# Performance work log

Measured on AMD Instinct MI355X. Metric: run time of the kernel, lower is better.

## Reference

```python
import jax, jax.numpy as jnp
import numpy as np

SCALING = 16.0 / 8.0  # alpha / rank
GAMMA = 1.0
EPS = 1e-12


def setup_inputs() -> dict:
    key = jax.random.key(0)
    ks = jax.random.split(key, 8)
    B, T, H, O = 4, 2048, 4096, 4096
    E_tot, E_act, r = 16, 4, 8
    return {
        "x": jax.random.normal(ks[0], (B, T, H), jnp.float32),
        "W_base": jax.random.normal(ks[1], (O, H), jnp.float32) * 0.02,
        "b_base": jax.random.normal(ks[2], (O,), jnp.float32) * 0.02,
        "lora_A": jax.random.normal(ks[3], (E_tot, r, H), jnp.float32) * 0.02,
        "lora_B": jax.random.normal(ks[4], (E_tot, O, r), jnp.float32) * 0.02,
        "router_W": jax.random.normal(ks[5], (E_tot, H), jnp.float32) * 0.02,
        "router_b": jax.random.normal(ks[6], (E_tot,), jnp.float32) * 0.02,
        "domain_prior": jax.random.uniform(ks[7], (E_tot,), jnp.float32),
        "active": jnp.arange(E_act, dtype=jnp.int32),
    }


def reference(x, W_base, b_base, lora_A, lora_B, router_W, router_b, domain_prior, active):
    # Base linear: [B,T,H] @ [H,O] -> [B,T,O]
    y = jnp.einsum('bth,oh->bto', x, W_base) + b_base
    # Gather active experts' low-rank factors
    A = lora_A[active]   # [E, r, H]
    Bm = lora_B[active]  # [E, O, r]
    # Grouped low-rank GEMMs (dropout is identity at inference)
    z = jnp.einsum('bth,erh->bter', x, A)            # [B,T,E,r]
    contribs = jnp.einsum('bter,eor->bteo', z, Bm) * SCALING  # [B,T,E,O]
    # Token router logits over all experts, restricted to active set
    logits = jnp.einsum('bth,eh->bte', x, router_W) + router_b  # [B,T,E_tot]
    logits = logits[..., active]                                 # [B,T,E]
    prior = domain_prior[active]                                 # [E]
    alpha = jax.nn.softmax(jnp.log(prior + EPS) + logits / GAMMA, axis=-1)  # [B,T,E]
    return y + jnp.einsum('bteo,bte->bto', contribs, alpha)
```

## Files before the change

### kernel.cpp

```cpp
#include <hip/hip_runtime.h>
#include <hip/hip_bf16.h>


typedef _Float16 f16x8 __attribute__((ext_vector_type(8)));
typedef float    f32x4 __attribute__((ext_vector_type(4)));

constexpr int H  = 4096;
constexpr int O  = 4096;
constexpr int KP = 4160;
constexpr int EA = 4;
constexpr float SCALING_F = 2.0f;

typedef const __attribute__((address_space(1))) void gvoid;
typedef __attribute__((address_space(3))) void svoid;

__device__ inline void gload16(const void* g, void* s) {
  __builtin_amdgcn_global_load_lds((gvoid*)g, (svoid*)s, 16, 0, 0);
}

__global__ __launch_bounds__(256) void convert_w3_kernel(
    const float* __restrict__ W, const float* __restrict__ lora_B,
    const float* __restrict__ lora_A, const float* __restrict__ router_W,
    const int* __restrict__ active, _Float16* __restrict__ wh,
    _Float16* __restrict__ vh) {
  const int bid = blockIdx.x;
  const int tid = threadIdx.x;
  if (bid < O) {
    const int o = bid;
    const float* wrow = W + (size_t)o * H;
    _Float16* dstrow = wh + (size_t)o * KP;
    for (int g = tid; g < 520; g += 256) {
      const int k = g * 8;
      float v[8];
      if (k < H) {
        float4 a = *(const float4*)(wrow + k), b = *(const float4*)(wrow + k + 4);
        v[0] = a.x; v[1] = a.y; v[2] = a.z; v[3] = a.w;
        v[4] = b.x; v[5] = b.y; v[6] = b.z; v[7] = b.w;
      } else if (k < H + 32) {
        const int e = (k - H) >> 3;
        const float* s = lora_B + ((size_t)active[e] * O + o) * 8;
        float4 a = *(const float4*)s, b = *(const float4*)(s + 4);
        v[0] = a.x; v[1] = a.y; v[2] = a.z; v[3] = a.w;
        v[4] = b.x; v[5] = b.y; v[6] = b.z; v[7] = b.w;
      } else {
#pragma unroll
        for (int i = 0; i < 8; ++i) v[i] = 0.f;
      }
      f16x8 h;
#pragma unroll
      for (int i = 0; i < 8; ++i) h[i] = (_Float16)v[i];
      *(f16x8*)(dstrow + k) = h;
    }
  } else {
    const int j = bid - O;
    const float* src = nullptr;
    if (j < 32)      src = lora_A + (size_t)(active[j >> 3] * 8 + (j & 7)) * H;
    else if (j < 36) src = router_W + (size_t)active[j - 32] * H;
    _Float16* dstrow = vh + (size_t)j * H;
    for (int g = tid; g < 512; g += 256) {
      const int k = g * 8;
      f16x8 h;
      if (src) {
        float4 a = *(const float4*)(src + k), b = *(const float4*)(src + k + 4);
        h[0] = (_Float16)a.x; h[1] = (_Float16)a.y;
        h[2] = (_Float16)a.z; h[3] = (_Float16)a.w;
        h[4] = (_Float16)b.x; h[5] = (_Float16)b.y;
        h[6] = (_Float16)b.z; h[7] = (_Float16)b.w;
      } else {
#pragma unroll
        for (int i = 0; i < 8; ++i) h[i] = (_Float16)0.f;
      }
      *(f16x8*)(dstrow + k) = h;
    }
  }
}

constexpr int RW5 = 16;

__global__ __launch_bounds__(1024) void router_fused5_kernel(
    const float* __restrict__ x, const _Float16* __restrict__ vh,
    const float* __restrict__ router_b, const float* __restrict__ prior,
    const int* __restrict__ active, _Float16* __restrict__ xh) {
  __shared__ float zred[RW5][16][48];
  const int tid  = threadIdx.x;
  const int lane = tid & 63;
  const int w    = tid >> 6;
  const long t0  = (long)blockIdx.x * 16;
  const int r15  = lane & 15;
  const int kg   = lane >> 4;

  const float*    xp  = x  + (t0 + r15) * H  + w * 256 + kg * 8;
  _Float16*       xhp = xh + (t0 + r15) * KP + w * 256 + kg * 8;
  const _Float16* vp  = vh + (size_t)r15 * H + w * 256 + kg * 8;

  f32x4 acc[3];
  const f32x4 zero = {0.f, 0.f, 0.f, 0.f};
  acc[0] = zero; acc[1] = zero; acc[2] = zero;

#pragma unroll
  for (int c = 0; c < 8; ++c) {
    const int ko = c * 32;
    float4 v0 = *(const float4*)(xp + ko);
    float4 v1 = *(const float4*)(xp + ko + 4);
    f16x8 a;
    a[0] = (_Float16)v0.x; a[1] = (_Float16)v0.y;
    a[2] = (_Float16)v0.z; a[3] = (_Float16)v0.w;
    a[4] = (_Float16)v1.x; a[5] = (_Float16)v1.y;
    a[6] = (_Float16)v1.z; a[7] = (_Float16)v1.w;
    *(f16x8*)(xhp + ko) = a;
#pragma unroll
    for (int nf = 0; nf < 3; ++nf) {
      f16x8 b = *(const f16x8*)(vp + (size_t)nf * 16 * H + ko);
      acc[nf] = __builtin_amdgcn_mfma_f32_16x16x32_f16(a, b, acc[nf], 0, 0, 0);
    }
  }

#pragma unroll
  for (int nf = 0; nf < 3; ++nf)
#pragma unroll
    for (int r = 0; r < 4; ++r)
      zred[w][kg * 4 + r][nf * 16 + r15] = acc[nf][r];
  __syncthreads();

  float s = 0.f;
  int tt = 0, jj = 0;
  if (tid < 16 * 48) {
    tt = tid / 48; jj = tid % 48;
#pragma unroll
    for (int ww = 0; ww < RW5; ++ww) s += zred[ww][tt][jj];
  }
  __syncthreads();
  if (tid < 16 * 48) zred[0][tt][jj] = s;
  __syncthreads();

  if (tid < 16 * EA) {
    const int t2 = tid >> 2, e = tid & 3;
    const float* zt = &zred[0][t2][0];
    float le[EA], mx = -1e30f;
#pragma unroll
    for (int e2 = 0; e2 < EA; ++e2) {
      const int ae = active[e2];
      le[e2] = logf(prior[ae] + 1e-12f) + zt[32 + e2] + router_b[ae];
      mx = fmaxf(mx, le[e2]);
    }
    float sum = 0.f;
#pragma unroll
    for (int e2 = 0; e2 < EA; ++e2) sum += expf(le[e2] - mx);
    const float a = expf(le[e] - mx) / sum * SCALING_F;
    f16x8 ch, zz;
#pragma unroll
    for (int r = 0; r < 8; ++r) {
      ch[r] = (_Float16)(a * zt[e * 8 + r]);
      zz[r] = (_Float16)0.f;
    }
    _Float16* xr = xh + (t0 + t2) * KP + H;
    *(f16x8*)(xr + e * 8) = ch;
    *(f16x8*)(xr + 32 + e * 8) = zz;
  }
}

constexpr int BM = 256, BN = 256, BK = 64, NT = KP / BK;

__global__ __launch_bounds__(512, 2) void gemm_kernel(
    const _Float16* __restrict__ xh, const _Float16* __restrict__ wh,
    const float* __restrict__ b_base, float* __restrict__ out) {
  __shared__ _Float16 As[2][BM * BK];
  __shared__ _Float16 Ws[2][BN * BK];
  const int tid  = threadIdx.x;
  const int lane = tid & 63;
  const int wave = tid >> 6;
  const int bid  = (int)blockIdx.x;
  const int im = bid >> 4;
  const int in = bid & 15;
  const size_t trow0 = (size_t)im * BM;
  const size_t ocol0 = (size_t)in * BN;
  const int wr = wave >> 2;
  const int wc = wave & 3;
  const int r15 = lane & 15;
  const int kg  = lane >> 4;

  f32x4 acc[8][4];
  const f32x4 zero = {0.f, 0.f, 0.f, 0.f};
#pragma unroll
  for (int m = 0; m < 8; ++m)
#pragma unroll
    for (int n = 0; n < 4; ++n) acc[m][n] = zero;

  auto stageA = [&](int s, int t, int h) {
#pragma unroll
    for (int i = 0; i < 2; ++i) {
      const int idx = tid + 512 * i;
      const int row = idx >> 3;
      const int sg  = (idx & 7) ^ (row & 7);
      gload16(xh + (trow0 + h * 128 + row) * KP + t * 64 + sg * 8,
              &As[s][h * 8192 + idx * 8]);
    }
  };
  auto stageB = [&](int s, int t, int h) {
#pragma unroll
    for (int i = 0; i < 2; ++i) {
      const int idx = tid + 512 * i;
      const int row = idx >> 3;
      const int sg  = (idx & 7) ^ (row & 7);
      gload16(wh + (ocol0 + h * 128 + row) * KP + t * 64 + sg * 8,
              &Ws[s][h * 8192 + idx * 8]);
    }
  };

  stageA(0, 0, 0); stageA(0, 0, 1);
  stageB(0, 0, 0); stageB(0, 0, 1);
  asm volatile("s_waitcnt vmcnt(0)" ::: "memory");
  __builtin_amdgcn_s_barrier();

  for (int t = 0; t < NT; ++t) {
    const int s = t & 1;
    const _Float16* Ab = &As[s][0];
    const _Float16* Bb = &Ws[s][0];
#pragma unroll
    for (int q = 0; q < 4; ++q) {
      const int mh = q >> 1, nh = q & 1;
      f16x8 af[4][2], bf[2][2];
#pragma unroll
      for (int m = 0; m < 4; ++m) {
        const int row = wr * 128 + (mh * 4 + m) * 16 + r15;
#pragma unroll
        for (int kk = 0; kk < 2; ++kk) {
          const int slot = (kk * 4 + kg) ^ (row & 7);
          af[m][kk] = *(const f16x8*)(Ab + row * 64 + slot * 8);
        }
      }
#pragma unroll
      for (int n = 0; n < 2; ++n) {
        const int row = wc * 64 + (nh * 2 + n) * 16 + r15;
#pragma unroll
        for (int kk = 0; kk < 2; ++kk) {
          const int slot = (kk * 4 + kg) ^ (row & 7);
          bf[n][kk] = *(const f16x8*)(Bb + row * 64 + slot * 8);
        }
      }
      if (t + 1 < NT) {
        if (q == 0)      { stageA(s ^ 1, t + 1, 0); stageA(s ^ 1, t + 1, 1); }
        else if (q == 1) { stageB(s ^ 1, t + 1, 0); stageB(s ^ 1, t + 1, 1); }
      }
      __builtin_amdgcn_s_barrier();
      asm volatile("s_waitcnt lgkmcnt(0)" ::: "memory");
      __builtin_amdgcn_sched_barrier(0);
      __builtin_amdgcn_s_setprio(1);
#pragma unroll
      for (int m = 0; m < 4; ++m)
#pragma unroll
        for (int n = 0; n < 2; ++n)
#pragma unroll
          for (int kk = 0; kk < 2; ++kk)
            acc[mh * 4 + m][nh * 2 + n] = __builtin_amdgcn_mfma_f32_16x16x32_f16(
                af[m][kk], bf[n][kk], acc[mh * 4 + m][nh * 2 + n], 0, 0, 0);
      __builtin_amdgcn_s_setprio(0);
      __builtin_amdgcn_sched_barrier(0);
      if (q == 3)
        asm volatile("s_waitcnt vmcnt(0)" ::: "memory");
      __builtin_amdgcn_s_barrier();
    }
  }

#pragma unroll
  for (int n = 0; n < 4; ++n) {
    const size_t col = ocol0 + wc * 64 + n * 16 + r15;
    const float bb = b_base[col];
#pragma unroll
    for (int m = 0; m < 8; ++m) {
      const size_t row = trow0 + wr * 128 + m * 16 + kg * 4;
#pragma unroll
      for (int j = 0; j < 4; ++j)
        out[(row + j) * O + col] = acc[m][n][j] + bb;
    }
  }
}

extern "C" void kernel_launch(void* const* d_in, const int* in_sizes, int n_in,
                              void* d_out, int out_size, void* d_ws, size_t ws_size,
                              hipStream_t stream) {
  const float* x        = (const float*)d_in[0];
  const float* W_base   = (const float*)d_in[1];
  const float* b_base   = (const float*)d_in[2];
  const float* lora_A   = (const float*)d_in[3];
  const float* lora_B   = (const float*)d_in[4];
  const float* router_W = (const float*)d_in[5];
  const float* router_b = (const float*)d_in[6];
  const float* prior    = (const float*)d_in[7];
  const int*   active   = (const int*)d_in[8];
  float* out = (float*)d_out;

  const int M = in_sizes[0] / H;

  char* ws = (char*)d_ws;
  _Float16* xh = (_Float16*)ws;
  _Float16* wh = (_Float16*)(ws + (size_t)M * KP * 2);
  _Float16* vh = (_Float16*)(ws + (size_t)M * KP * 2 + (size_t)O * KP * 2);

  convert_w3_kernel<<<O + 48, 256, 0, stream>>>(W_base, lora_B, lora_A, router_W,
                                                active, wh, vh);
  router_fused5_kernel<<<M / 16, 1024, 0, stream>>>(x, vh, router_b, prior, active, xh);
  gemm_kernel<<<(M / BM) * (O / BN), 512, 0, stream>>>(xh, wh, b_base, out);
}
```

Before: 616.0 us.

## Switch GEMM to 256x128 tiles with triple-buffered LDS prefetch

Halves the N tile to 128, doubling the block count, and moves from double to triple buffering so loads for tile t+2 are issued while tile t computes, with partial vmcnt waits. The goal is to hide global-load latency and give better wave balance across CUs. The cost is lower reuse per tile, meaning more global/LDS traffic per MFMA, and larger LDS use per block. The epilogue is reorganized to match the narrower tile.

```diff
diff --git a/kernel.cpp b/kernel.cpp
--- a/kernel.cpp
+++ b/kernel.cpp
@@ -159,19 +159,19 @@
   }
 }
 
-constexpr int BM = 256, BN = 256, BK = 64, NT = KP / BK;
-
-__global__ __launch_bounds__(512, 2) void gemm_kernel(
+constexpr int BM = 256, BN = 128, BK = 64, NT = KP / BK;
+
+__global__ __launch_bounds__(512) void gemm_kernel(
     const _Float16* __restrict__ xh, const _Float16* __restrict__ wh,
     const float* __restrict__ b_base, float* __restrict__ out) {
-  __shared__ _Float16 As[2][BM * BK];
-  __shared__ _Float16 Ws[2][BN * BK];
+  __shared__ _Float16 As[3][BM * BK];
+  __shared__ _Float16 Ws[3][BN * BK];
   const int tid  = threadIdx.x;
   const int lane = tid & 63;
   const int wave = tid >> 6;
   const int bid  = (int)blockIdx.x;
-  const int im = bid >> 4;
-  const int in = bid & 15;
+  const int im = bid >> 5;
+  const int in = bid & 31;
   const size_t trow0 = (size_t)im * BM;
   const size_t ocol0 = (size_t)in * BN;
   const int wr = wave >> 2;
@@ -179,12 +179,12 @@
   const int r15 = lane & 15;
   const int kg  = lane >> 4;
 
-  f32x4 acc[8][4];
+  f32x4 acc[8][2];
   const f32x4 zero = {0.f, 0.f, 0.f, 0.f};
 #pragma unroll
   for (int m = 0; m < 8; ++m)
 #pragma unroll
-    for (int n = 0; n < 4; ++n) acc[m][n] = zero;
+    for (int n = 0; n < 2; ++n) acc[m][n] = zero;
 
   auto stageA = [&](int s, int t, int h) {
 #pragma unroll
@@ -196,33 +196,32 @@
               &As[s][h * 8192 + idx * 8]);
     }
   };
-  auto stageB = [&](int s, int t, int h) {
+  auto stageB = [&](int s, int t) {
 #pragma unroll
     for (int i = 0; i < 2; ++i) {
       const int idx = tid + 512 * i;
       const int row = idx >> 3;
       const int sg  = (idx & 7) ^ (row & 7);
-      gload16(wh + (ocol0 + h * 128 + row) * KP + t * 64 + sg * 8,
-              &Ws[s][h * 8192 + idx * 8]);
+      gload16(wh + (ocol0 + row) * KP + t * 64 + sg * 8, &Ws[s][idx * 8]);
     }
   };
 
-  stageA(0, 0, 0); stageA(0, 0, 1);
-  stageB(0, 0, 0); stageB(0, 0, 1);
-  asm volatile("s_waitcnt vmcnt(0)" ::: "memory");
+  stageA(0, 0, 0); stageA(0, 0, 1); stageB(0, 0);
+  stageA(1, 1, 0); stageA(1, 1, 1); stageB(1, 1);
+  asm volatile("s_waitcnt vmcnt(6)" ::: "memory");
   __builtin_amdgcn_s_barrier();
 
   for (int t = 0; t < NT; ++t) {
-    const int s = t & 1;
+    const int s  = t % 3;
+    const int s2 = (t + 2) % 3;
     const _Float16* Ab = &As[s][0];
     const _Float16* Bb = &Ws[s][0];
 #pragma unroll
-    for (int q = 0; q < 4; ++q) {
-      const int mh = q >> 1, nh = q & 1;
+    for (int q = 0; q < 2; ++q) {
       f16x8 af[4][2], bf[2][2];
 #pragma unroll
       for (int m = 0; m < 4; ++m) {
-        const int row = wr * 128 + (mh * 4 + m) * 16 + r15;
+        const int row = wr * 128 + (q * 4 + m) * 16 + r15;
 #pragma unroll
         for (int kk = 0; kk < 2; ++kk) {
           const int slot = (kk * 4 + kg) ^ (row & 7);
@@ -231,16 +230,16 @@
       }
 #pragma unroll
       for (int n = 0; n < 2; ++n) {
-        const int row = wc * 64 + (nh * 2 + n) * 16 + r15;
+        const int row = wc * 32 + n * 16 + r15;
 #pragma unroll
         for (int kk = 0; kk < 2; ++kk) {
           const int slot = (kk * 4 + kg) ^ (row & 7);
           bf[n][kk] = *(const f16x8*)(Bb + row * 64 + slot * 8);
         }
       }
-      if (t + 1 < NT) {
-        if (q == 0)      { stageA(s ^ 1, t + 1, 0); stageA(s ^ 1, t + 1, 1); }
-        else if (q == 1) { stageB(s ^ 1, t + 1, 0); stageB(s ^ 1, t + 1, 1); }
+      if (t + 2 < NT) {
+        if (q == 0) { stageA(s2, t + 2, 0); stageA(s2, t + 2, 1); }
+        else        { stageB(s2, t + 2); }
       }
       __builtin_amdgcn_s_barrier();
       asm volatile("s_waitcnt lgkmcnt(0)" ::: "memory");
@@ -252,26 +251,35 @@
         for (int n = 0; n < 2; ++n)
 #pragma unroll
           for (int kk = 0; kk < 2; ++kk)
-            acc[mh * 4 + m][nh * 2 + n] = __builtin_amdgcn_mfma_f32_16x16x32_f16(
-                af[m][kk], bf[n][kk], acc[mh * 4 + m][nh * 2 + n], 0, 0, 0);
+            acc[q * 4 + m][n] = __builtin_amdgcn_mfma_f32_16x16x32_f16(
+                af[m][kk], bf[n][kk], acc[q * 4 + m][n], 0, 0, 0);
       __builtin_amdgcn_s_setprio(0);
       __builtin_amdgcn_sched_barrier(0);
-      if (q == 3)
-        asm volatile("s_waitcnt vmcnt(0)" ::: "memory");
+      if (q == 1) {
+        if (t < NT - 2)
+          asm volatile("s_waitcnt vmcnt(6)" ::: "memory");
+        else if (t == NT - 2)
+          asm volatile("s_waitcnt vmcnt(0)" ::: "memory");
+      }
       __builtin_amdgcn_s_barrier();
     }
   }
 
 #pragma unroll
-  for (int n = 0; n < 4; ++n) {
-    const size_t col = ocol0 + wc * 64 + n * 16 + r15;
-    const float bb = b_base[col];
-#pragma unroll
-    for (int m = 0; m < 8; ++m) {
-      const size_t row = trow0 + wr * 128 + m * 16 + kg * 4;
-#pragma unroll
-      for (int j = 0; j < 4; ++j)
-        out[(row + j) * O + col] = acc[m][n][j] + bb;
+  for (int n = 0; n < 2; ++n) {
+  }
+  float bb[2];
+#pragma unroll
+  for (int n = 0; n < 2; ++n) bb[n] = b_base[ocol0 + wc * 32 + n * 16 + r15];
+#pragma unroll
+  for (int m = 0; m < 8; ++m) {
+    const size_t row = trow0 + wr * 128 + m * 16 + kg * 4;
+#pragma unroll
+    for (int j = 0; j < 4; ++j) {
+      float* orow = out + (row + j) * O + ocol0 + wc * 32 + r15;
+#pragma unroll
+      for (int n = 0; n < 2; ++n)
+        orow[n * 16] = acc[m][n][j] + bb[n];
     }
   }
 }
```

After: 620.6 us. Within noise of the previous version (+0.8%).
